# Kernel optimization log

Hardware: AMD Instinct MI355X
Metric: run time of the kernel (lower is better)

Reference implementation:

```python
import jax, jax.numpy as jnp
import numpy as np

N, E, IN, H, OUT, K = 50000, 800000, 128, 128, 40, 10
ALPHA, EPS, AH = 0.1, 1e-5, 64


def setup_inputs() -> dict:
    key = jax.random.key(0)
    ks = jax.random.split(key, 32)
    rn = lambda k, s, sc=0.05: jax.random.normal(k, s, jnp.float32) * sc
    return dict(
        x=jax.random.normal(ks[0], (N, IN), jnp.float32),
        edge_index=jax.random.randint(ks[1], (2, E), 0, N, jnp.int64),
        edge_weight=jax.random.uniform(ks[2], (E,), jnp.float32),
        lin1_w=rn(ks[3], (H, IN)), lin1_b=rn(ks[4], (H,)),
        bn1_g=jnp.ones((H,), jnp.float32), bn1_b=jnp.zeros((H,), jnp.float32),
        bn1_m=rn(ks[5], (H,)), bn1_v=jax.random.uniform(ks[6], (H,), jnp.float32, 0.5, 1.5),
        lin2_w=rn(ks[7], (H, H)), lin2_b=rn(ks[8], (H,)),
        bn2_g=jnp.ones((H,), jnp.float32), bn2_b=jnp.zeros((H,), jnp.float32),
        bn2_m=rn(ks[9], (H,)), bn2_v=jax.random.uniform(ks[10], (H,), jnp.float32, 0.5, 1.5),
        att1_w=rn(ks[11], (AH, 2 * H)), att1_b=rn(ks[12], (AH,)),
        att2_w=rn(ks[13], (K + 1, AH)), att2_b=rn(ks[14], (K + 1,)),
        head1_w=rn(ks[15], (H // 2, H)), head1_b=rn(ks[16], (H // 2,)),
        bn3_g=jnp.ones((H // 2,), jnp.float32), bn3_b=jnp.zeros((H // 2,), jnp.float32),
        bn3_m=rn(ks[17], (H // 2,)), bn3_v=jax.random.uniform(ks[18], (H // 2,), jnp.float32, 0.5, 1.5),
        head2_w=rn(ks[19], (OUT, H // 2)), head2_b=rn(ks[20], (OUT,)),
    )


def _bn(x, g, b, m, v):
    # eval-mode BatchNorm1d with running stats
    return (x - m) * jax.lax.rsqrt(v + EPS) * g + b


def reference(x, edge_index, edge_weight,
              lin1_w, lin1_b, bn1_g, bn1_b, bn1_m, bn1_v,
              lin2_w, lin2_b, bn2_g, bn2_b, bn2_m, bn2_v,
              att1_w, att1_b, att2_w, att2_b,
              head1_w, head1_b, bn3_g, bn3_b, bn3_m, bn3_v,
              head2_w, head2_b):
    row, col = edge_index[0], edge_index[1]

    # dense stem (dropout is identity in eval mode)
    h = jax.nn.relu(_bn(x @ lin1_w.T + lin1_b, bn1_g, bn1_b, bn1_m, bn1_v))
    identity = h
    h = jax.nn.relu(_bn(h @ lin2_w.T + lin2_b, bn2_g, bn2_b, bn2_m, bn2_v)) + identity
    base = h  # h0 for APPNP

    # edge normalization (loop-invariant): w_e / clamp(sum_w(row), 1)
    wsum = jnp.clip(jax.ops.segment_sum(edge_weight, row, num_segments=N), 1.0)
    enorm = edge_weight / wsum[row]  # [E]

    xs = [h]
    for _ in range(K):  # fixed K iterations of gather -> scatter-add
        agg = jax.ops.segment_sum(h[row] * enorm[:, None], col, num_segments=N)
        h = (1.0 - ALPHA) * agg + ALPHA * base
        xs.append(h)

    stacked = jnp.stack(xs, axis=-1)                    # [N, H, K+1]
    ctx = jnp.concatenate([xs[0], xs[-1]], axis=-1)     # [N, 2H]
    a = jax.nn.gelu(ctx @ att1_w.T + att1_b, approximate=False) @ att2_w.T + att2_b
    w = jax.nn.softmax(a, axis=-1)[:, None, :]          # [N, 1, K+1]
    fused = (stacked * w).sum(axis=-1)                  # [N, H]

    z = jax.nn.relu(_bn(fused @ head1_w.T + head1_b, bn3_g, bn3_b, bn3_m, bn3_v))
    return z @ head2_w.T + head2_b
```

## Files before the change

### kernel.cpp

```cpp
#include <hip/hip_runtime.h>
#include <hip/hip_fp16.h>
#include <math.h>

#define NN 50000
#define EE 800000
#define HH 128
#define KIT 10
#define NHF (NN * HH)
#define CC 64
#define CH 12500
#define RRH 4
#define NRH 12500

typedef _Float16 half8 __attribute__((ext_vector_type(8)));
typedef _Float16 half4v __attribute__((ext_vector_type(4)));
typedef float floatx4 __attribute__((ext_vector_type(4)));

static_assert(NN % 16 == 0, "row tiles must be exact");

__device__ __forceinline__ float gelu_exact(float x) {
  return 0.5f * x * (1.f + erff(x * 0.70710678118654752f));
}

__device__ __forceinline__ float4 ld4(const float* p) { return *(const float4*)p; }
__device__ __forceinline__ float4 ld4(const __half* p) {
  const __half2* q = (const __half2*)p;
  float2 lo = __half22float2(q[0]);
  float2 hi = __half22float2(q[1]);
  return make_float4(lo.x, lo.y, hi.x, hi.y);
}
__device__ __forceinline__ void st1(float* p, float v) { *p = v; }
__device__ __forceinline__ void st1(__half* p, float v) { *p = __float2half_rn(v); }

__global__ __launch_bounds__(256) void hist2_kernel(const int* __restrict__ ei,
                                                    const float* __restrict__ ew,
                                                    int* __restrict__ pdeg,
                                                    float* __restrict__ pwsum,
                                                    int* __restrict__ rank) {
  __shared__ int hist[NRH];
  const int c = blockIdx.x;
  const int z = blockIdx.y;
  const bool isdeg = (z < RRH);
  const int lo = (isdeg ? z : z - RRH) * NRH;
  for (int i = threadIdx.x; i < NRH; i += 256) hist[i] = 0;
  __syncthreads();
  const int e0 = c * CH;
  if (isdeg) {
    const int4* d4 = (const int4*)(ei + (size_t)EE + e0);
    for (int i = threadIdx.x; i < CH / 4; i += 256) {
      int4 d = d4[i];
      int e = e0 + i * 4;
      unsigned u0 = (unsigned)(d.x - lo), u1 = (unsigned)(d.y - lo);
      unsigned u2 = (unsigned)(d.z - lo), u3 = (unsigned)(d.w - lo);
      if (u0 < NRH) rank[e]     = atomicAdd(&hist[u0], 1);
      if (u1 < NRH) rank[e + 1] = atomicAdd(&hist[u1], 1);
      if (u2 < NRH) rank[e + 2] = atomicAdd(&hist[u2], 1);
      if (u3 < NRH) rank[e + 3] = atomicAdd(&hist[u3], 1);
    }
    __syncthreads();
    for (int i = threadIdx.x; i < NRH; i += 256)
      pdeg[(size_t)c * NN + lo + i] = hist[i];
  } else {
    float* whist = (float*)hist;
    const int4* s4 = (const int4*)(ei + e0);
    const float4* w4 = (const float4*)(ew + e0);
    for (int i = threadIdx.x; i < CH / 4; i += 256) {
      int4 s = s4[i];
      float4 w = w4[i];
      unsigned u0 = (unsigned)(s.x - lo), u1 = (unsigned)(s.y - lo);
      unsigned u2 = (unsigned)(s.z - lo), u3 = (unsigned)(s.w - lo);
      if (u0 < NRH) atomicAdd(&whist[u0], w.x);
      if (u1 < NRH) atomicAdd(&whist[u1], w.y);
      if (u2 < NRH) atomicAdd(&whist[u2], w.z);
      if (u3 < NRH) atomicAdd(&whist[u3], w.w);
    }
    __syncthreads();
    for (int i = threadIdx.x; i < NRH; i += 256)
      pwsum[(size_t)c * NN + lo + i] = whist[i];
  }
}

__global__ __launch_bounds__(256) void reduce_kernel(int* __restrict__ pdeg,
                                                     const float* __restrict__ pwsum,
                                                     int* __restrict__ deg,
                                                     float* __restrict__ wsum,
                                                     int* __restrict__ bsum) {
  int node = blockIdx.x * 256 + threadIdx.x;
  int acc = 0; float wacc = 0.f;
  if (node < NN) {
    for (int c = 0; c < CC; ++c) {
      size_t idx = (size_t)c * NN + node;
      int t = pdeg[idx];
      pdeg[idx] = acc;
      acc += t;
      wacc += pwsum[idx];
    }
    deg[node] = acc;
    wsum[node] = wacc;
  }
  __shared__ int red[256];
  red[threadIdx.x] = (node < NN) ? acc : 0;
  __syncthreads();
  for (int off = 128; off > 0; off >>= 1) {
    if (threadIdx.x < off) red[threadIdx.x] += red[threadIdx.x + off];
    __syncthreads();
  }
  if (threadIdx.x == 0) bsum[blockIdx.x] = red[0];
}

__global__ __launch_bounds__(256) void scan2_kernel(const int* __restrict__ bsum,
                                                    int* __restrict__ boff,
                                                    int* __restrict__ row_start, int nb, int n) {
  __shared__ int buf[256];
  int tid = threadIdx.x;
  int v = (tid < nb) ? bsum[tid] : 0;
  buf[tid] = v;
  __syncthreads();
  for (int off = 1; off < 256; off <<= 1) {
    int t = (tid >= off) ? buf[tid - off] : 0;
    __syncthreads();
    buf[tid] += t;
    __syncthreads();
  }
  if (tid < nb) boff[tid] = buf[tid] - v;
  if (tid == 255) row_start[n] = buf[255];
}

__global__ __launch_bounds__(256) void scan3_kernel(const int* __restrict__ deg,
                                                    const int* __restrict__ boff,
                                                    int* __restrict__ row_start, int n) {
  __shared__ int buf[256];
  int tid = threadIdx.x;
  int i = blockIdx.x * 256 + tid;
  int v = (i < n) ? deg[i] : 0;
  buf[tid] = v;
  __syncthreads();
  for (int off = 1; off < 256; off <<= 1) {
    int t = (tid >= off) ? buf[tid - off] : 0;
    __syncthreads();
    buf[tid] += t;
    __syncthreads();
  }
  if (i < n) row_start[i] = boff[blockIdx.x] + buf[tid] - v;
}

__global__ __launch_bounds__(256) void csr_fill_kernel(const int* __restrict__ ei,
                                                       const float* __restrict__ ew,
                                                       const float* __restrict__ wsum,
                                                       const int* __restrict__ row_start,
                                                       const int* __restrict__ pdeg_excl,
                                                       const int* __restrict__ rank,
                                                       int2* __restrict__ csr, int e_cnt) {
  int e = blockIdx.x * 256 + threadIdx.x;
  if (e >= e_cnt) return;
  int c = e / CH;
  int src = ei[e], dst = ei[EE + e];
  float ws = wsum[src];
  ws = ws < 1.f ? 1.f : ws;
  float v = 0.9f * ew[e] / ws;
  int pos = row_start[dst] + pdeg_excl[(size_t)c * NN + dst] + rank[e];
  csr[pos] = make_int2(src, __float_as_int(v));
}

__global__ __launch_bounds__(256) void prop_kernel(const __half* __restrict__ h_cur,
                                                   const __half* __restrict__ base,
                                                   const int* __restrict__ row_start,
                                                   const long* __restrict__ csr,
                                                   __half* __restrict__ h_next) {
  int node = __builtin_amdgcn_readfirstlane((int)blockIdx.x * 4 + (int)(threadIdx.x >> 6));
  if (node >= NN) return;
  int lane = threadIdx.x & 63;
  const __half2* hc = (const __half2*)h_cur;
  float2 b = __half22float2(((const __half2*)base)[(size_t)node * 64 + lane]);
  float ax = 0.1f * b.x, ay = 0.1f * b.y;
  float bx = 0.f, by = 0.f;
  int s = row_start[node], e = row_start[node + 1];
  int nfull = (e - s) >> 3;
  int i = s;
  if (nfull > 0) {
    long cur[8];
#pragma unroll
    for (int j = 0; j < 8; ++j) cur[j] = csr[i + j];
    i += 8;
    for (int bidx = 1; bidx < nfull; ++bidx) {
      long nxt[8];
#pragma unroll
      for (int j = 0; j < 8; ++j) nxt[j] = csr[i + j];
      i += 8;
      float2 g[8];
#pragma unroll
      for (int j = 0; j < 8; ++j) g[j] = __half22float2(hc[(size_t)(int)cur[j] * 64 + lane]);
#pragma unroll
      for (int j = 0; j < 8; ++j) {
        float v = __int_as_float((int)(cur[j] >> 32));
        if (j & 1) { bx = fmaf(v, g[j].x, bx); by = fmaf(v, g[j].y, by); }
        else       { ax = fmaf(v, g[j].x, ax); ay = fmaf(v, g[j].y, ay); }
      }
#pragma unroll
      for (int j = 0; j < 8; ++j) cur[j] = nxt[j];
    }
    float2 g[8];
#pragma unroll
    for (int j = 0; j < 8; ++j) g[j] = __half22float2(hc[(size_t)(int)cur[j] * 64 + lane]);
#pragma unroll
    for (int j = 0; j < 8; ++j) {
      float v = __int_as_float((int)(cur[j] >> 32));
      if (j & 1) { bx = fmaf(v, g[j].x, bx); by = fmaf(v, g[j].y, by); }
      else       { ax = fmaf(v, g[j].x, ax); ay = fmaf(v, g[j].y, ay); }
    }
  }
  for (; i < e; ++i) {
    long c0 = csr[i];
    float2 g0 = __half22float2(hc[(size_t)(int)c0 * 64 + lane]);
    float v = __int_as_float((int)(c0 >> 32));
    ax = fmaf(v, g0.x, ax); ay = fmaf(v, g0.y, ay);
  }
  ((__half2*)h_next)[(size_t)node * 64 + lane] =
      __float22half2_rn(make_float2(ax + bx, ay + by));
}

template <int K, int KA, int JP, int JR, int ACT, bool RESID, typename IT, typename OT>
__global__ __launch_bounds__(256) void mfma_dense2(
    const IT* __restrict__ Xa, const IT* __restrict__ Xb,
    const float* __restrict__ W, const float* __restrict__ lb,
    const float* __restrict__ bg, const float* __restrict__ bb,
    const float* __restrict__ bm, const float* __restrict__ bv,
    const OT* __restrict__ resid, OT* __restrict__ out) {
  static_assert(K % 32 == 0 && KA % 32 == 0 && JP % 16 == 0, "");
  constexpr int JT = JP / 16;
  constexpr int NS = K / 32;
  constexpr bool ISF = __is_same(IT, float);
  __shared__ _Float16 wL[JP][K];

  const int tid = threadIdx.x;
  const int wv = tid >> 6, lane = tid & 63;
  const int q = lane >> 4, m = lane & 15;
  const int t = blockIdx.x * 4 + wv;
  const bool active = (t < NN / 16);
  const int row = t * 16 + m;

  half8  a[ISF ? 1 : NS];
  float4 af0[ISF ? NS : 1], af1[ISF ? NS : 1];
  if (active) {
#pragma unroll
    for (int s = 0; s < NS; ++s) {
      int c = s * 32 + q * 8;
      if constexpr (ISF) {
        const float* p = (const float*)Xa + (size_t)row * K + c;
        af0[s] = *(const float4*)p;
        af1[s] = *(const float4*)(p + 4);
      } else {
        const __half* p = (c < KA) ? (const __half*)Xa + (size_t)row * KA + c
                                   : (const __half*)Xb + (size_t)row * (K - KA) + (c - KA);
        a[s] = *(const half8*)p;
      }
    }
  }

  constexpr int C4 = K / 4;
  for (int idx = tid; idx < JP * C4; idx += 256) {
    int j = idx / C4;
    int c4 = (idx % C4) * 4;
    float4 v = make_float4(0.f, 0.f, 0.f, 0.f);
    if (j < JR) v = *(const float4*)&W[(size_t)j * K + c4];
    int cs = ((((c4 >> 3) ^ (j & 7)) << 3) | (c4 & 7));
    *(half4v*)&wL[j][cs] = (half4v){(_Float16)v.x, (_Float16)v.y,
                                    (_Float16)v.z, (_Float16)v.w};
  }
  __syncthreads();

  if (!active) return;

  floatx4 acc[JT];
#pragma unroll
  for (int jt = 0; jt < JT; ++jt) acc[jt] = (floatx4)(0.f);

#pragma unroll
  for (int s = 0; s < NS; ++s) {
    half8 av;
    if constexpr (ISF) {
      float4 f0 = af0[s], f1 = af1[s];
      av = (half8){(_Float16)f0.x, (_Float16)f0.y, (_Float16)f0.z, (_Float16)f0.w,
                   (_Float16)f1.x, (_Float16)f1.y, (_Float16)f1.z, (_Float16)f1.w};
    } else {
      av = a[s];
    }
    int kq = s * 4 + q;
#pragma unroll
    for (int jt = 0; jt < JT; ++jt) {
      int j = jt * 16 + m;
      half8 b = *(const half8*)&wL[j][(kq ^ (j & 7)) << 3];
      acc[jt] = __builtin_amdgcn_mfma_f32_16x16x32_f16(av, b, acc[jt], 0, 0, 0);
    }
  }

#pragma unroll
  for (int jt = 0; jt < JT; ++jt) {
    int j = jt * 16 + m;
    if (j >= JR) continue;
    float sc = 0.f, sh;
    if (ACT == 1) {
      sc = bg[j] * rsqrtf(bv[j] + 1e-5f);
      sh = (lb[j] - bm[j]) * sc + bb[j];
    } else {
      sh = lb[j];
    }
#pragma unroll
    for (int reg = 0; reg < 4; ++reg) {
      int r = t * 16 + q * 4 + reg;
      float aa = acc[jt][reg];
      float y;
      if (ACT == 0)      y = aa + sh;
      else if (ACT == 1) y = fmaxf(fmaf(aa, sc, sh), 0.f);
      else               y = gelu_exact(aa + sh);
      if (RESID) y += (float)resid[(size_t)r * JR + j];
      st1(&out[(size_t)r * JR + j], y);
    }
  }
}

__global__ __launch_bounds__(64) void att2_softmax_kernel(const __half* __restrict__ g,
                                                          const float* __restrict__ W2,
                                                          const float* __restrict__ b2,
                                                          float* __restrict__ attw, int n_rows) {
  __shared__ float gl[64][65];
  int r0 = blockIdx.x * 64;
  for (int idx = threadIdx.x; idx < 64 * 16; idx += 64) {
    int r = idx >> 4, c4 = (idx & 15) * 4;
    float4 v = make_float4(0.f, 0.f, 0.f, 0.f);
    if (r0 + r < n_rows) v = ld4(&g[(size_t)(r0 + r) * 64 + c4]);
    gl[r][c4] = v.x; gl[r][c4 + 1] = v.y; gl[r][c4 + 2] = v.z; gl[r][c4 + 3] = v.w;
  }
  __syncthreads();
  int r = threadIdx.x;
  int n = r0 + r;
  if (n >= n_rows) return;
  float a[KIT + 1];
#pragma unroll
  for (int j = 0; j < KIT + 1; ++j) {
    float acc = b2[j];
#pragma unroll
    for (int k = 0; k < 64; ++k) acc = fmaf(gl[r][k], W2[j * 64 + k], acc);
    a[j] = acc;
  }
  float mx = a[0];
#pragma unroll
  for (int j = 1; j < KIT + 1; ++j) mx = fmaxf(mx, a[j]);
  float s = 0.f;
#pragma unroll
  for (int j = 0; j < KIT + 1; ++j) { a[j] = expf(a[j] - mx); s += a[j]; }
  float inv = 1.f / s;
#pragma unroll
  for (int j = 0; j < KIT + 1; ++j) attw[n * 16 + j] = a[j] * inv;
}

__global__ __launch_bounds__(256) void fused_gather_kernel(const __half* __restrict__ XS,
                                                           const float* __restrict__ attw,
                                                           __half* __restrict__ fused) {
  int node = __builtin_amdgcn_readfirstlane((int)blockIdx.x * 4 + (int)(threadIdx.x >> 6));
  if (node >= NN) return;
  int lane = threadIdx.x & 63;
  float ax = 0.f, ay = 0.f;
#pragma unroll
  for (int k = 0; k <= KIT; ++k) {
    float wk = attw[node * 16 + k];
    float2 v = __half22float2(((const __half2*)(XS + (size_t)k * NHF))[(size_t)node * 64 + lane]);
    ax = fmaf(wk, v.x, ax);
    ay = fmaf(wk, v.y, ay);
  }
  ((__half2*)fused)[(size_t)node * 64 + lane] = __float22half2_rn(make_float2(ax, ay));
}

__global__ __launch_bounds__(256) void fused_accum_kernel(const __half* __restrict__ h,
                                                          const float* __restrict__ attw,
                                                          float* __restrict__ fused, int k) {
  int node = __builtin_amdgcn_readfirstlane((int)blockIdx.x * 4 + (int)(threadIdx.x >> 6));
  if (node >= NN) return;
  int lane = threadIdx.x & 63;
  float wk = attw[node * 16 + k];
  float2 v = __half22float2(((const __half2*)h)[(size_t)node * 64 + lane]);
  float2 o;
  if (k == 0) {
    o = make_float2(wk * v.x, wk * v.y);
  } else {
    float2 f = ((const float2*)fused)[(size_t)node * 64 + lane];
    o = make_float2(fmaf(wk, v.x, f.x), fmaf(wk, v.y, f.y));
  }
  ((float2*)fused)[(size_t)node * 64 + lane] = o;
}

extern "C" void kernel_launch(void* const* d_in, const int* in_sizes, int n_in,
                              void* d_out, int out_size, void* d_ws, size_t ws_size,
                              hipStream_t stream) {
  (void)in_sizes; (void)n_in; (void)out_size;
  const float* x      = (const float*)d_in[0];
  const int*   ei     = (const int*)d_in[1];
  const float* ew     = (const float*)d_in[2];
  const float* lin1_w = (const float*)d_in[3];
  const float* lin1_b = (const float*)d_in[4];
  const float* bn1_g  = (const float*)d_in[5];
  const float* bn1_b  = (const float*)d_in[6];
  const float* bn1_m  = (const float*)d_in[7];
  const float* bn1_v  = (const float*)d_in[8];
  const float* lin2_w = (const float*)d_in[9];
  const float* lin2_b = (const float*)d_in[10];
  const float* bn2_g  = (const float*)d_in[11];
  const float* bn2_b  = (const float*)d_in[12];
  const float* bn2_m  = (const float*)d_in[13];
  const float* bn2_v  = (const float*)d_in[14];
  const float* att1_w = (const float*)d_in[15];
  const float* att1_b = (const float*)d_in[16];
  const float* att2_w = (const float*)d_in[17];
  const float* att2_b = (const float*)d_in[18];
  const float* head1_w= (const float*)d_in[19];
  const float* head1_b= (const float*)d_in[20];
  const float* bn3_g  = (const float*)d_in[21];
  const float* bn3_b  = (const float*)d_in[22];
  const float* bn3_m  = (const float*)d_in[23];
  const float* bn3_v  = (const float*)d_in[24];
  const float* head2_w= (const float*)d_in[25];
  const float* head2_b= (const float*)d_in[26];
  float* out = (float*)d_out;

  char* p = (char*)d_ws;
  auto alloc = [&](size_t bytes) -> void* {
    void* r = (void*)p;
    p += (bytes + 255) & ~(size_t)255;
    return r;
  };
  int*   row_start= (int*)alloc((size_t)(NN + 1) * 4);
  int*   bsum     = (int*)alloc((size_t)256 * 4);
  int*   boff     = (int*)alloc((size_t)256 * 4);
  int*   deg      = (int*)alloc((size_t)NN * 4);
  float* wsum     = (float*)alloc((size_t)NN * 4);
  long*  csr      = (long*)alloc((size_t)EE * 8);
  __half* gbuf    = (__half*)alloc((size_t)NN * 64 * 2);
  float* attw     = (float*)alloc((size_t)NN * 16 * 4);
  __half* h1      = (__half*)alloc((size_t)NHF * 2);
  __half* fusedH  = (__half*)alloc((size_t)NHF * 2);
  __half* zbuf    = (__half*)alloc((size_t)NN * 64 * 2);
  size_t common = (size_t)(p - (char*)d_ws);
  size_t stored_need = common + (size_t)(KIT + 1) * NHF * 2 + 4096;
  bool stored = ws_size >= stored_need;

  __half* XS = nullptr;
  int* pdeg; float* pwsum; int* rank;
  if (stored) {
    XS = (__half*)alloc((size_t)(KIT + 1) * NHF * 2);
    char* ovl = (char*)(XS + (size_t)8 * NHF);
    pdeg  = (int*)ovl;
    pwsum = (float*)(ovl + (size_t)CC * NN * 4);
    rank  = (int*)(ovl + 2 * (size_t)CC * NN * 4);
  } else {
    pdeg  = (int*)alloc((size_t)CC * NN * 4);
    pwsum = (float*)alloc((size_t)CC * NN * 4);
    rank  = (int*)alloc((size_t)EE * 4);
  }

  const int GE  = (EE + 255) / 256;
  const int GN  = (NN + 255) / 256;
  const int GT  = (NN / 16 + 3) / 4;
  const int GP  = (NN + 3) / 4;
  const int GA  = (NN + 63) / 64;

  hist2_kernel<<<dim3(CC, 2 * RRH), 256, 0, stream>>>(ei, ew, pdeg, pwsum, rank);
  reduce_kernel<<<GN, 256, 0, stream>>>(pdeg, pwsum, deg, wsum, bsum);
  scan2_kernel<<<1, 256, 0, stream>>>(bsum, boff, row_start, GN, NN);
  scan3_kernel<<<GN, 256, 0, stream>>>(deg, boff, row_start, NN);
  csr_fill_kernel<<<GE, 256, 0, stream>>>(ei, ew, wsum, row_start, pdeg, rank,
                                          (int2*)csr, EE);

  if (stored) {
    mfma_dense2<128, 128, 128, 128, 1, false, float, __half><<<GT, 256, 0, stream>>>(
        x, (const float*)nullptr, lin1_w, lin1_b, bn1_g, bn1_b, bn1_m, bn1_v, nullptr, h1);
    mfma_dense2<128, 128, 128, 128, 1, true, __half, __half><<<GT, 256, 0, stream>>>(
        h1, (const __half*)nullptr, lin2_w, lin2_b, bn2_g, bn2_b, bn2_m, bn2_v, h1, XS);
    for (int k = 0; k < KIT; ++k) {
      prop_kernel<<<GP, 256, 0, stream>>>(XS + (size_t)k * NHF, XS, row_start,
                                          csr, XS + (size_t)(k + 1) * NHF);
    }
    mfma_dense2<256, 128, 64, 64, 2, false, __half, __half><<<GT, 256, 0, stream>>>(
        XS, XS + (size_t)KIT * NHF, att1_w, att1_b, nullptr, nullptr, nullptr, nullptr,
        nullptr, gbuf);
    att2_softmax_kernel<<<GA, 64, 0, stream>>>(gbuf, att2_w, att2_b, attw, NN);
    fused_gather_kernel<<<GP, 256, 0, stream>>>(XS, attw, fusedH);
    mfma_dense2<128, 128, 64, 64, 1, false, __half, __half><<<GT, 256, 0, stream>>>(
        fusedH, (const __half*)nullptr, head1_w, head1_b, bn3_g, bn3_b, bn3_m, bn3_v,
        nullptr, zbuf);
  } else {
    float*  fusedF = (float*)alloc((size_t)NHF * 4);
    __half* base   = (__half*)alloc((size_t)NHF * 2);
    __half* hA     = (__half*)alloc((size_t)NHF * 2);
    __half* hB     = (__half*)alloc((size_t)NHF * 2);
    mfma_dense2<128, 128, 128, 128, 1, false, float, __half><<<GT, 256, 0, stream>>>(
        x, (const float*)nullptr, lin1_w, lin1_b, bn1_g, bn1_b, bn1_m, bn1_v, nullptr, h1);
    mfma_dense2<128, 128, 128, 128, 1, true, __half, __half><<<GT, 256, 0, stream>>>(
        h1, (const __half*)nullptr, lin2_w, lin2_b, bn2_g, bn2_b, bn2_m, bn2_v, h1, base);
    const __half* cur = base;
    for (int k = 1; k <= KIT; ++k) {
      __half* nxt = (k & 1) ? hA : hB;
      prop_kernel<<<GP, 256, 0, stream>>>(cur, base, row_start, csr, nxt);
      cur = nxt;
    }
    mfma_dense2<256, 128, 64, 64, 2, false, __half, __half><<<GT, 256, 0, stream>>>(
        base, cur, att1_w, att1_b, nullptr, nullptr, nullptr, nullptr, nullptr, gbuf);
    att2_softmax_kernel<<<GA, 64, 0, stream>>>(gbuf, att2_w, att2_b, attw, NN);
    fused_accum_kernel<<<GP, 256, 0, stream>>>(base, attw, fusedF, 0);
    cur = base;
    for (int k = 1; k <= KIT; ++k) {
      __half* nxt = (k & 1) ? hA : hB;
      prop_kernel<<<GP, 256, 0, stream>>>(cur, base, row_start, csr, nxt);
      fused_accum_kernel<<<GP, 256, 0, stream>>>(nxt, attw, fusedF, k);
      cur = nxt;
    }
    mfma_dense2<128, 128, 64, 64, 1, false, float, __half><<<GT, 256, 0, stream>>>(
        fusedF, (const float*)nullptr, head1_w, head1_b, bn3_g, bn3_b, bn3_m, bn3_v,
        nullptr, zbuf);
  }

  mfma_dense2<64, 64, 48, 40, 0, false, __half, float><<<GT, 256, 0, stream>>>(
      zbuf, (const __half*)nullptr, head2_w, head2_b, nullptr, nullptr, nullptr, nullptr,
      nullptr, out);
}
```

Baseline: 574.4 us.

## Pad CSR rows to multiples of eight and process two nodes per wavefront

```diff
diff --git a/kernel.cpp b/kernel.cpp
--- a/kernel.cpp
+++ b/kernel.cpp
@@ -99,7 +99,7 @@
     wsum[node] = wacc;
   }
   __shared__ int red[256];
-  red[threadIdx.x] = (node < NN) ? acc : 0;
+  red[threadIdx.x] = (node < NN) ? ((acc + 7) & ~7) : 0;
   __syncthreads();
   for (int off = 128; off > 0; off >>= 1) {
     if (threadIdx.x < off) red[threadIdx.x] += red[threadIdx.x + off];
@@ -132,7 +132,7 @@
   __shared__ int buf[256];
   int tid = threadIdx.x;
   int i = blockIdx.x * 256 + tid;
-  int v = (i < n) ? deg[i] : 0;
+  int v = (i < n) ? ((deg[i] + 7) & ~7) : 0;
   buf[tid] = v;
   __syncthreads();
   for (int off = 1; off < 256; off <<= 1) {
@@ -162,61 +162,93 @@
   csr[pos] = make_int2(src, __float_as_int(v));
 }
 
-__global__ __launch_bounds__(256) void prop_kernel(const __half* __restrict__ h_cur,
-                                                   const __half* __restrict__ base,
-                                                   const int* __restrict__ row_start,
-                                                   const long* __restrict__ csr,
-                                                   __half* __restrict__ h_next) {
-  int node = __builtin_amdgcn_readfirstlane((int)blockIdx.x * 4 + (int)(threadIdx.x >> 6));
+__global__ __launch_bounds__(256) void pad_fill_kernel(const int* __restrict__ deg,
+                                                       const int* __restrict__ row_start,
+                                                       long* __restrict__ csr) {
+  int node = blockIdx.x * 256 + threadIdx.x;
   if (node >= NN) return;
+  int s = row_start[node] + deg[node];
+  int e = row_start[node + 1];
+  for (int i = s; i < e; ++i) csr[i] = 0;
+}
+
+__global__ __launch_bounds__(256, 6) void prop_kernel(const __half* __restrict__ h_cur,
+                                                      const __half* __restrict__ base,
+                                                      const int* __restrict__ row_start,
+                                                      const long* __restrict__ csr,
+                                                      __half* __restrict__ h_next) {
+  int pair = __builtin_amdgcn_readfirstlane((int)blockIdx.x * 4 + (int)(threadIdx.x >> 6));
+  int nA = pair * 2;
+  if (nA >= NN) return;
+  int nB = nA + 1;
   int lane = threadIdx.x & 63;
   const __half2* hc = (const __half2*)h_cur;
-  float2 b = __half22float2(((const __half2*)base)[(size_t)node * 64 + lane]);
-  float ax = 0.1f * b.x, ay = 0.1f * b.y;
-  float bx = 0.f, by = 0.f;
-  int s = row_start[node], e = row_start[node + 1];
-  int nfull = (e - s) >> 3;
+  float2 vbA = __half22float2(((const __half2*)base)[(size_t)nA * 64 + lane]);
+  float2 vbB = __half22float2(((const __half2*)base)[(size_t)nB * 64 + lane]);
+  float aAx = 0.1f * vbA.x, aAy = 0.1f * vbA.y, bAx = 0.f, bAy = 0.f;
+  float aBx = 0.1f * vbB.x, aBy = 0.1f * vbB.y, bBx = 0.f, bBy = 0.f;
+  int s  = __builtin_amdgcn_readfirstlane(row_start[nA]);
+  int eA = __builtin_amdgcn_readfirstlane(row_start[nA + 1]);
+  int eB = __builtin_amdgcn_readfirstlane(row_start[nB + 1]);
+  int nb = (eB - s) >> 3;
   int i = s;
-  if (nfull > 0) {
+  if (nb > 0) {
     long cur[8];
+    bool curB = (i >= eA);
 #pragma unroll
     for (int j = 0; j < 8; ++j) cur[j] = csr[i + j];
     i += 8;
-    for (int bidx = 1; bidx < nfull; ++bidx) {
+    for (int bidx = 1; bidx < nb; ++bidx) {
       long nxt[8];
+      bool nxtB = (i >= eA);
 #pragma unroll
       for (int j = 0; j < 8; ++j) nxt[j] = csr[i + j];
       i += 8;
       float2 g[8];
 #pragma unroll
       for (int j = 0; j < 8; ++j) g[j] = __half22float2(hc[(size_t)(int)cur[j] * 64 + lane]);
+      if (curB) {
+#pragma unroll
+        for (int j = 0; j < 8; ++j) {
+          float v = __int_as_float((int)(cur[j] >> 32));
+          if (j & 1) { bBx = fmaf(v, g[j].x, bBx); bBy = fmaf(v, g[j].y, bBy); }
+          else       { aBx = fmaf(v, g[j].x, aBx); aBy = fmaf(v, g[j].y, aBy); }
+        }
+      } else {
+#pragma unroll
+        for (int j = 0; j < 8; ++j) {
+          float v = __int_as_float((int)(cur[j] >> 32));
+          if (j & 1) { bAx = fmaf(v, g[j].x, bAx); bAy = fmaf(v, g[j].y, bAy); }
+          else       { aAx = fmaf(v, g[j].x, aAx); aAy = fmaf(v, g[j].y, aAy); }
+        }
+      }
+#pragma unroll
+      for (int j = 0; j < 8; ++j) cur[j] = nxt[j];
+      curB = nxtB;
+    }
+    float2 g[8];
+#pragma unroll
+    for (int j = 0; j < 8; ++j) g[j] = __half22float2(hc[(size_t)(int)cur[j] * 64 + lane]);
+    if (curB) {
 #pragma unroll
       for (int j = 0; j < 8; ++j) {
         float v = __int_as_float((int)(cur[j] >> 32));
-        if (j & 1) { bx = fmaf(v, g[j].x, bx); by = fmaf(v, g[j].y, by); }
-        else       { ax = fmaf(v, g[j].x, ax); ay = fmaf(v, g[j].y, ay); }
+        if (j & 1) { bBx = fmaf(v, g[j].x, bBx); bBy = fmaf(v, g[j].y, bBy); }
+        else       { aBx = fmaf(v, g[j].x, aBx); aBy = fmaf(v, g[j].y, aBy); }
       }
-#pragma unroll
-      for (int j = 0; j < 8; ++j) cur[j] = nxt[j];
-    }
-    float2 g[8];
-#pragma unroll
-    for (int j = 0; j < 8; ++j) g[j] = __half22float2(hc[(size_t)(int)cur[j] * 64 + lane]);
-#pragma unroll
-    for (int j = 0; j < 8; ++j) {
-      float v = __int_as_float((int)(cur[j] >> 32));
-      if (j & 1) { bx = fmaf(v, g[j].x, bx); by = fmaf(v, g[j].y, by); }
-      else       { ax = fmaf(v, g[j].x, ax); ay = fmaf(v, g[j].y, ay); }
-    }
-  }
-  for (; i < e; ++i) {
-    long c0 = csr[i];
-    float2 g0 = __half22float2(hc[(size_t)(int)c0 * 64 + lane]);
-    float v = __int_as_float((int)(c0 >> 32));
-    ax = fmaf(v, g0.x, ax); ay = fmaf(v, g0.y, ay);
-  }
-  ((__half2*)h_next)[(size_t)node * 64 + lane] =
-      __float22half2_rn(make_float2(ax + bx, ay + by));
+    } else {
+#pragma unroll
+      for (int j = 0; j < 8; ++j) {
+        float v = __int_as_float((int)(cur[j] >> 32));
+        if (j & 1) { bAx = fmaf(v, g[j].x, bAx); bAy = fmaf(v, g[j].y, bAy); }
+        else       { aAx = fmaf(v, g[j].x, aAx); aAy = fmaf(v, g[j].y, aAy); }
+      }
+    }
+  }
+  ((__half2*)h_next)[(size_t)nA * 64 + lane] =
+      __float22half2_rn(make_float2(aAx + bAx, aAy + bAy));
+  ((__half2*)h_next)[(size_t)nB * 64 + lane] =
+      __float22half2_rn(make_float2(aBx + bBx, aBy + bBy));
 }
 
 template <int K, int KA, int JP, int JR, int ACT, bool RESID, typename IT, typename OT>
@@ -433,7 +465,7 @@
   int*   boff     = (int*)alloc((size_t)256 * 4);
   int*   deg      = (int*)alloc((size_t)NN * 4);
   float* wsum     = (float*)alloc((size_t)NN * 4);
-  long*  csr      = (long*)alloc((size_t)EE * 8);
+  long*  csr      = (long*)alloc(((size_t)EE + 8 * NN) * 8);
   __half* gbuf    = (__half*)alloc((size_t)NN * 64 * 2);
   float* attw     = (float*)alloc((size_t)NN * 16 * 4);
   __half* h1      = (__half*)alloc((size_t)NHF * 2);
@@ -461,6 +493,7 @@
   const int GN  = (NN + 255) / 256;
   const int GT  = (NN / 16 + 3) / 4;
   const int GP  = (NN + 3) / 4;
+  const int GP2 = (NN / 2 + 3) / 4;
   const int GA  = (NN + 63) / 64;
 
   hist2_kernel<<<dim3(CC, 2 * RRH), 256, 0, stream>>>(ei, ew, pdeg, pwsum, rank);
@@ -469,6 +502,7 @@
   scan3_kernel<<<GN, 256, 0, stream>>>(deg, boff, row_start, NN);
   csr_fill_kernel<<<GE, 256, 0, stream>>>(ei, ew, wsum, row_start, pdeg, rank,
                                           (int2*)csr, EE);
+  pad_fill_kernel<<<GN, 256, 0, stream>>>(deg, row_start, csr);
 
   if (stored) {
     mfma_dense2<128, 128, 128, 128, 1, false, float, __half><<<GT, 256, 0, stream>>>(
@@ -476,8 +510,8 @@
     mfma_dense2<128, 128, 128, 128, 1, true, __half, __half><<<GT, 256, 0, stream>>>(
         h1, (const __half*)nullptr, lin2_w, lin2_b, bn2_g, bn2_b, bn2_m, bn2_v, h1, XS);
     for (int k = 0; k < KIT; ++k) {
-      prop_kernel<<<GP, 256, 0, stream>>>(XS + (size_t)k * NHF, XS, row_start,
-                                          csr, XS + (size_t)(k + 1) * NHF);
+      prop_kernel<<<GP2, 256, 0, stream>>>(XS + (size_t)k * NHF, XS, row_start,
+                                           csr, XS + (size_t)(k + 1) * NHF);
     }
     mfma_dense2<256, 128, 64, 64, 2, false, __half, __half><<<GT, 256, 0, stream>>>(
         XS, XS + (size_t)KIT * NHF, att1_w, att1_b, nullptr, nullptr, nullptr, nullptr,
@@ -499,7 +533,7 @@
     const __half* cur = base;
     for (int k = 1; k <= KIT; ++k) {
       __half* nxt = (k & 1) ? hA : hB;
-      prop_kernel<<<GP, 256, 0, stream>>>(cur, base, row_start, csr, nxt);
+      prop_kernel<<<GP2, 256, 0, stream>>>(cur, base, row_start, csr, nxt);
       cur = nxt;
     }
     mfma_dense2<256, 128, 64, 64, 2, false, __half, __half><<<GT, 256, 0, stream>>>(
@@ -509,7 +543,7 @@
     cur = base;
     for (int k = 1; k <= KIT; ++k) {
       __half* nxt = (k & 1) ? hA : hB;
-      prop_kernel<<<GP, 256, 0, stream>>>(cur, base, row_start, csr, nxt);
+      prop_kernel<<<GP2, 256, 0, stream>>>(cur, base, row_start, csr, nxt);
       fused_accum_kernel<<<GP, 256, 0, stream>>>(nxt, attw, fusedF, k);
       cur = nxt;
     }
```

After: 564.9 us. About the same (-1.7%).

## Split feature vectors into 32-column planes and propagate plane-by-plane with padded CSR

Applied to the files above, without the earlier changes.

```diff
diff --git a/kernel.cpp b/kernel.cpp
--- a/kernel.cpp
+++ b/kernel.cpp
@@ -11,6 +11,7 @@
 #define CH 12500
 #define RRH 4
 #define NRH 12500
+#define GPROP 1536
 
 typedef _Float16 half8 __attribute__((ext_vector_type(8)));
 typedef _Float16 half4v __attribute__((ext_vector_type(4)));
@@ -99,7 +100,7 @@
     wsum[node] = wacc;
   }
   __shared__ int red[256];
-  red[threadIdx.x] = (node < NN) ? acc : 0;
+  red[threadIdx.x] = (node < NN) ? ((acc + 7) & ~7) : 0;
   __syncthreads();
   for (int off = 128; off > 0; off >>= 1) {
     if (threadIdx.x < off) red[threadIdx.x] += red[threadIdx.x + off];
@@ -132,7 +133,7 @@
   __shared__ int buf[256];
   int tid = threadIdx.x;
   int i = blockIdx.x * 256 + tid;
-  int v = (i < n) ? deg[i] : 0;
+  int v = (i < n) ? ((deg[i] + 7) & ~7) : 0;
   buf[tid] = v;
   __syncthreads();
   for (int off = 1; off < 256; off <<= 1) {
@@ -162,64 +163,103 @@
   csr[pos] = make_int2(src, __float_as_int(v));
 }
 
-__global__ __launch_bounds__(256) void prop_kernel(const __half* __restrict__ h_cur,
-                                                   const __half* __restrict__ base,
-                                                   const int* __restrict__ row_start,
-                                                   const long* __restrict__ csr,
-                                                   __half* __restrict__ h_next) {
-  int node = __builtin_amdgcn_readfirstlane((int)blockIdx.x * 4 + (int)(threadIdx.x >> 6));
+__global__ __launch_bounds__(256) void pad_fill_kernel(const int* __restrict__ deg,
+                                                       const int* __restrict__ row_start,
+                                                       long* __restrict__ csr) {
+  int node = blockIdx.x * 256 + threadIdx.x;
   if (node >= NN) return;
-  int lane = threadIdx.x & 63;
-  const __half2* hc = (const __half2*)h_cur;
-  float2 b = __half22float2(((const __half2*)base)[(size_t)node * 64 + lane]);
-  float ax = 0.1f * b.x, ay = 0.1f * b.y;
-  float bx = 0.f, by = 0.f;
-  int s = row_start[node], e = row_start[node + 1];
-  int nfull = (e - s) >> 3;
-  int i = s;
-  if (nfull > 0) {
-    long cur[8];
-#pragma unroll
-    for (int j = 0; j < 8; ++j) cur[j] = csr[i + j];
-    i += 8;
-    for (int bidx = 1; bidx < nfull; ++bidx) {
-      long nxt[8];
-#pragma unroll
-      for (int j = 0; j < 8; ++j) nxt[j] = csr[i + j];
-      i += 8;
-      float2 g[8];
-#pragma unroll
-      for (int j = 0; j < 8; ++j) g[j] = __half22float2(hc[(size_t)(int)cur[j] * 64 + lane]);
-#pragma unroll
-      for (int j = 0; j < 8; ++j) {
-        float v = __int_as_float((int)(cur[j] >> 32));
-        if (j & 1) { bx = fmaf(v, g[j].x, bx); by = fmaf(v, g[j].y, by); }
-        else       { ax = fmaf(v, g[j].x, ax); ay = fmaf(v, g[j].y, ay); }
+  int s = row_start[node] + deg[node];
+  int e = row_start[node + 1];
+  for (int i = s; i < e; ++i) csr[i] = 0;
+}
+
+#define SELFMA(CEV, VV, IO)                                                        \
+  {                                                                                \
+    float w_ = __int_as_float((int)((CEV) >> 32));                                 \
+    int sel_ = ((IO) >= e1) + ((IO) >= e2) + ((IO) >= e3);                         \
+    if (sel_ == 0)      { acc0.x = fmaf(w_, (VV).x, acc0.x); acc0.y = fmaf(w_, (VV).y, acc0.y); } \
+    else if (sel_ == 1) { acc1.x = fmaf(w_, (VV).x, acc1.x); acc1.y = fmaf(w_, (VV).y, acc1.y); } \
+    else if (sel_ == 2) { acc2.x = fmaf(w_, (VV).x, acc2.x); acc2.y = fmaf(w_, (VV).y, acc2.y); } \
+    else                { acc3.x = fmaf(w_, (VV).x, acc3.x); acc3.y = fmaf(w_, (VV).y, acc3.y); } \
+  }
+
+__global__ __launch_bounds__(256, 6) void prop_plane_kernel(
+    const __half* __restrict__ h_cur, const __half* __restrict__ base,
+    const int* __restrict__ row_start, const long* __restrict__ csr,
+    __half* __restrict__ h_next) {
+  const int W = GPROP * 4;
+  const int wid = (int)blockIdx.x * 4 + (int)(threadIdx.x >> 6);
+  const int lane = threadIdx.x & 63;
+  const int g = lane >> 4, l = lane & 15;
+  const int UNITS = NN / 4;
+
+  for (int plane = 0; plane < 4; ++plane) {
+    const __half2* hp = (const __half2*)(h_cur + (size_t)plane * NN * 32);
+    const __half2* bp = (const __half2*)(base + (size_t)plane * NN * 32);
+    __half2* np = (__half2*)(h_next + (size_t)plane * NN * 32);
+    for (int u = wid; u < UNITS; u += W) {
+      int n0 = u * 4;
+      int s  = __builtin_amdgcn_readfirstlane(row_start[n0]);
+      int e1 = __builtin_amdgcn_readfirstlane(row_start[n0 + 1]);
+      int e2 = __builtin_amdgcn_readfirstlane(row_start[n0 + 2]);
+      int e3 = __builtin_amdgcn_readfirstlane(row_start[n0 + 3]);
+      int e4 = __builtin_amdgcn_readfirstlane(row_start[n0 + 4]);
+      float2 acc0 = make_float2(0.f, 0.f), acc1 = make_float2(0.f, 0.f);
+      float2 acc2 = make_float2(0.f, 0.f), acc3 = make_float2(0.f, 0.f);
+      int nb = (e4 - s) >> 2;
+      int nfull = nb >> 2;
+      int i = s, ic = s;
+      if (nfull > 0) {
+        long cur[4];
+#pragma unroll
+        for (int j = 0; j < 4; ++j) cur[j] = csr[i + j * 4 + g];
+        i += 16;
+        for (int b = 1; b < nfull; ++b) {
+          long nxt[4];
+#pragma unroll
+          for (int j = 0; j < 4; ++j) nxt[j] = csr[i + j * 4 + g];
+          i += 16;
+          float2 v[4];
+#pragma unroll
+          for (int j = 0; j < 4; ++j)
+            v[j] = __half22float2(hp[(size_t)(int)cur[j] * 16 + l]);
+#pragma unroll
+          for (int j = 0; j < 4; ++j) SELFMA(cur[j], v[j], ic + j * 4);
+#pragma unroll
+          for (int j = 0; j < 4; ++j) cur[j] = nxt[j];
+          ic += 16;
+        }
+        float2 v[4];
+#pragma unroll
+        for (int j = 0; j < 4; ++j)
+          v[j] = __half22float2(hp[(size_t)(int)cur[j] * 16 + l]);
+#pragma unroll
+        for (int j = 0; j < 4; ++j) SELFMA(cur[j], v[j], ic + j * 4);
+        ic += 16;
       }
-#pragma unroll
-      for (int j = 0; j < 8; ++j) cur[j] = nxt[j];
-    }
-    float2 g[8];
-#pragma unroll
-    for (int j = 0; j < 8; ++j) g[j] = __half22float2(hc[(size_t)(int)cur[j] * 64 + lane]);
-#pragma unroll
-    for (int j = 0; j < 8; ++j) {
-      float v = __int_as_float((int)(cur[j] >> 32));
-      if (j & 1) { bx = fmaf(v, g[j].x, bx); by = fmaf(v, g[j].y, by); }
-      else       { ax = fmaf(v, g[j].x, ax); ay = fmaf(v, g[j].y, ay); }
-    }
-  }
-  for (; i < e; ++i) {
-    long c0 = csr[i];
-    float2 g0 = __half22float2(hc[(size_t)(int)c0 * 64 + lane]);
-    float v = __int_as_float((int)(c0 >> 32));
-    ax = fmaf(v, g0.x, ax); ay = fmaf(v, g0.y, ay);
-  }
-  ((__half2*)h_next)[(size_t)node * 64 + lane] =
-      __float22half2_rn(make_float2(ax + bx, ay + by));
-}
-
-template <int K, int KA, int JP, int JR, int ACT, bool RESID, typename IT, typename OT>
+      for (; i < e4; i += 4) {
+        long ce = csr[i + g];
+        float2 v = __half22float2(hp[(size_t)(int)ce * 16 + l]);
+        SELFMA(ce, v, i);
+      }
+      acc0.x += __shfl_xor(acc0.x, 16); acc0.y += __shfl_xor(acc0.y, 16);
+      acc0.x += __shfl_xor(acc0.x, 32); acc0.y += __shfl_xor(acc0.y, 32);
+      acc1.x += __shfl_xor(acc1.x, 16); acc1.y += __shfl_xor(acc1.y, 16);
+      acc1.x += __shfl_xor(acc1.x, 32); acc1.y += __shfl_xor(acc1.y, 32);
+      acc2.x += __shfl_xor(acc2.x, 16); acc2.y += __shfl_xor(acc2.y, 16);
+      acc2.x += __shfl_xor(acc2.x, 32); acc2.y += __shfl_xor(acc2.y, 32);
+      acc3.x += __shfl_xor(acc3.x, 16); acc3.y += __shfl_xor(acc3.y, 16);
+      acc3.x += __shfl_xor(acc3.x, 32); acc3.y += __shfl_xor(acc3.y, 32);
+      float2 r = (g == 0) ? acc0 : (g == 1) ? acc1 : (g == 2) ? acc2 : acc3;
+      float2 bb = __half22float2(bp[(size_t)(n0 + g) * 16 + l]);
+      np[(size_t)(n0 + g) * 16 + l] = __float22half2_rn(
+          make_float2(fmaf(0.1f, bb.x, r.x), fmaf(0.1f, bb.y, r.y)));
+    }
+  }
+}
+
+template <int K, int KA, int JP, int JR, int ACT, bool RESID, typename IT, typename OT,
+          bool PIN = false, bool POUT = false>
 __global__ __launch_bounds__(256) void mfma_dense2(
     const IT* __restrict__ Xa, const IT* __restrict__ Xb,
     const float* __restrict__ W, const float* __restrict__ lb,
@@ -249,6 +289,11 @@
         const float* p = (const float*)Xa + (size_t)row * K + c;
         af0[s] = *(const float4*)p;
         af1[s] = *(const float4*)(p + 4);
+      } else if constexpr (PIN) {
+        int cc = (c < KA) ? c : c - KA;
+        const __half* Xp = (c < KA) ? (const __half*)Xa : (const __half*)Xb;
+        const __half* p = Xp + (size_t)(cc >> 5) * (NN * 32) + (size_t)row * 32 + (cc & 31);
+        a[s] = *(const half8*)p;
       } else {
         const __half* p = (c < KA) ? (const __half*)Xa + (size_t)row * KA + c
                                    : (const __half*)Xb + (size_t)row * (K - KA) + (c - KA);
@@ -314,7 +359,10 @@
       else if (ACT == 1) y = fmaxf(fmaf(aa, sc, sh), 0.f);
       else               y = gelu_exact(aa + sh);
       if (RESID) y += (float)resid[(size_t)r * JR + j];
-      st1(&out[(size_t)r * JR + j], y);
+      if constexpr (POUT)
+        st1(&out[(size_t)(j >> 5) * (NN * 32) + (size_t)r * 32 + (j & 31)], y);
+      else
+        st1(&out[(size_t)r * JR + j], y);
     }
   }
 }
@@ -360,11 +408,13 @@
   int node = __builtin_amdgcn_readfirstlane((int)blockIdx.x * 4 + (int)(threadIdx.x >> 6));
   if (node >= NN) return;
   int lane = threadIdx.x & 63;
+  int q = lane >> 4, l = lane & 15;
+  size_t pidx = (size_t)q * (NN * 16) + (size_t)node * 16 + l;
   float ax = 0.f, ay = 0.f;
 #pragma unroll
   for (int k = 0; k <= KIT; ++k) {
     float wk = attw[node * 16 + k];
-    float2 v = __half22float2(((const __half2*)(XS + (size_t)k * NHF))[(size_t)node * 64 + lane]);
+    float2 v = __half22float2(((const __half2*)(XS + (size_t)k * NHF))[pidx]);
     ax = fmaf(wk, v.x, ax);
     ay = fmaf(wk, v.y, ay);
   }
@@ -377,8 +427,10 @@
   int node = __builtin_amdgcn_readfirstlane((int)blockIdx.x * 4 + (int)(threadIdx.x >> 6));
   if (node >= NN) return;
   int lane = threadIdx.x & 63;
+  int q = lane >> 4, l = lane & 15;
   float wk = attw[node * 16 + k];
-  float2 v = __half22float2(((const __half2*)h)[(size_t)node * 64 + lane]);
+  float2 v = __half22float2(
+      ((const __half2*)h)[(size_t)q * (NN * 16) + (size_t)node * 16 + l]);
   float2 o;
   if (k == 0) {
     o = make_float2(wk * v.x, wk * v.y);
@@ -433,7 +485,7 @@
   int*   boff     = (int*)alloc((size_t)256 * 4);
   int*   deg      = (int*)alloc((size_t)NN * 4);
   float* wsum     = (float*)alloc((size_t)NN * 4);
-  long*  csr      = (long*)alloc((size_t)EE * 8);
+  long*  csr      = (long*)alloc(((size_t)EE + 8 * NN) * 8);
   __half* gbuf    = (__half*)alloc((size_t)NN * 64 * 2);
   float* attw     = (float*)alloc((size_t)NN * 16 * 4);
   __half* h1      = (__half*)alloc((size_t)NHF * 2);
@@ -469,17 +521,20 @@
   scan3_kernel<<<GN, 256, 0, stream>>>(deg, boff, row_start, NN);
   csr_fill_kernel<<<GE, 256, 0, stream>>>(ei, ew, wsum, row_start, pdeg, rank,
                                           (int2*)csr, EE);
+  pad_fill_kernel<<<GN, 256, 0, stream>>>(deg, row_start, csr);
 
   if (stored) {
     mfma_dense2<128, 128, 128, 128, 1, false, float, __half><<<GT, 256, 0, stream>>>(
         x, (const float*)nullptr, lin1_w, lin1_b, bn1_g, bn1_b, bn1_m, bn1_v, nullptr, h1);
-    mfma_dense2<128, 128, 128, 128, 1, true, __half, __half><<<GT, 256, 0, stream>>>(
+    mfma_dense2<128, 128, 128, 128, 1, true, __half, __half, false, true>
+        <<<GT, 256, 0, stream>>>(
         h1, (const __half*)nullptr, lin2_w, lin2_b, bn2_g, bn2_b, bn2_m, bn2_v, h1, XS);
     for (int k = 0; k < KIT; ++k) {
-      prop_kernel<<<GP, 256, 0, stream>>>(XS + (size_t)k * NHF, XS, row_start,
-                                          csr, XS + (size_t)(k + 1) * NHF);
-    }
-    mfma_dense2<256, 128, 64, 64, 2, false, __half, __half><<<GT, 256, 0, stream>>>(
+      prop_plane_kernel<<<GPROP, 256, 0, stream>>>(XS + (size_t)k * NHF, XS, row_start,
+                                                   csr, XS + (size_t)(k + 1) * NHF);
+    }
+    mfma_dense2<256, 128, 64, 64, 2, false, __half, __half, true, false>
+        <<<GT, 256, 0, stream>>>(
         XS, XS + (size_t)KIT * NHF, att1_w, att1_b, nullptr, nullptr, nullptr, nullptr,
         nullptr, gbuf);
     att2_softmax_kernel<<<GA, 64, 0, stream>>>(gbuf, att2_w, att2_b, attw, NN);
@@ -494,22 +549,24 @@
     __half* hB     = (__half*)alloc((size_t)NHF * 2);
     mfma_dense2<128, 128, 128, 128, 1, false, float, __half><<<GT, 256, 0, stream>>>(
         x, (const float*)nullptr, lin1_w, lin1_b, bn1_g, bn1_b, bn1_m, bn1_v, nullptr, h1);
-    mfma_dense2<128, 128, 128, 128, 1, true, __half, __half><<<GT, 256, 0, stream>>>(
+    mfma_dense2<128, 128, 128, 128, 1, true, __half, __half, false, true>
+        <<<GT, 256, 0, stream>>>(
         h1, (const __half*)nullptr, lin2_w, lin2_b, bn2_g, bn2_b, bn2_m, bn2_v, h1, base);
     const __half* cur = base;
     for (int k = 1; k <= KIT; ++k) {
       __half* nxt = (k & 1) ? hA : hB;
-      prop_kernel<<<GP, 256, 0, stream>>>(cur, base, row_start, csr, nxt);
+      prop_plane_kernel<<<GPROP, 256, 0, stream>>>(cur, base, row_start, csr, nxt);
       cur = nxt;
     }
-    mfma_dense2<256, 128, 64, 64, 2, false, __half, __half><<<GT, 256, 0, stream>>>(
+    mfma_dense2<256, 128, 64, 64, 2, false, __half, __half, true, false>
+        <<<GT, 256, 0, stream>>>(
         base, cur, att1_w, att1_b, nullptr, nullptr, nullptr, nullptr, nullptr, gbuf);
     att2_softmax_kernel<<<GA, 64, 0, stream>>>(gbuf, att2_w, att2_b, attw, NN);
     fused_accum_kernel<<<GP, 256, 0, stream>>>(base, attw, fusedF, 0);
     cur = base;
     for (int k = 1; k <= KIT; ++k) {
       __half* nxt = (k & 1) ? hA : hB;
-      prop_kernel<<<GP, 256, 0, stream>>>(cur, base, row_start, csr, nxt);
+      prop_plane_kernel<<<GPROP, 256, 0, stream>>>(cur, base, row_start, csr, nxt);
       fused_accum_kernel<<<GP, 256, 0, stream>>>(nxt, attw, fusedF, k);
       cur = nxt;
     }
```

After: 949.2 us. +65.2%, slower.
